# Optimization experiments

Measured on AMD Instinct MI355X. Metric: run time of the kernel, lower is better.

The kernel has to match this reference:

```python
import jax, jax.numpy as jnp
import numpy as np

N = 100_000      # nodes
E = 6_400_000    # directed edges (avg degree 64)
F_IN, H, F_OUT = 128, 16, 64


def setup_inputs() -> dict:
    key = jax.random.key(0)
    k1, k2, k3, k4 = jax.random.split(key, 4)
    x = jax.random.normal(k1, (N, F_IN), dtype=jnp.float32)
    edge_index = jax.random.randint(k2, (2, E), 0, N, dtype=jnp.int32)
    # Glorot-ish init for the two GCNConv weight matrices
    W1 = jax.random.normal(k3, (F_IN, H), dtype=jnp.float32) * (1.0 / np.sqrt(F_IN))
    b1 = jnp.zeros((H,), dtype=jnp.float32)
    W2 = jax.random.normal(k4, (H, F_OUT), dtype=jnp.float32) * (1.0 / np.sqrt(H))
    b2 = jnp.zeros((F_OUT,), dtype=jnp.float32)
    return {"x": x, "edge_index": edge_index, "W1": W1, "b1": b1, "W2": W2, "b2": b2}


def _gcn_conv(x, src, dst, norm, W, b):
    # PyG GCNConv: transform first (small hidden dim), then normalized scatter-add
    h = x @ W                                  # [N, d_out]
    msg = h[src] * norm[:, None]               # gather + scale, [E+N, d_out]
    agg = jax.ops.segment_sum(msg, dst, num_segments=N)
    return agg + b


def reference(x, edge_index, W1, b1, W2, b2):
    src, dst = edge_index[0], edge_index[1]
    # add self-loops (GCNConv default add_self_loops=True)
    loop = jnp.arange(N, dtype=src.dtype)
    src = jnp.concatenate([src, loop])
    dst = jnp.concatenate([dst, loop])
    # symmetric normalization D^{-1/2} (A+I) D^{-1/2}
    deg = jax.ops.segment_sum(jnp.ones(src.shape[0], x.dtype), dst, num_segments=N)
    dinv = jax.lax.rsqrt(jnp.maximum(deg, 1e-12))  # deg >= 1 thanks to self-loops
    norm = dinv[src] * dinv[dst]                   # [E+N]
    h = jax.nn.relu(_gcn_conv(x, src, dst, norm, W1, b1))
    return _gcn_conv(h, src, dst, norm, W2, b2)
```

## Files before the change

### kernel.cpp

```cpp
#include <hip/hip_runtime.h>
#include <hip/hip_fp16.h>

constexpr int NN   = 100000;
constexpr int EE   = 6400000;
constexpr int FIN  = 128;
constexpr int HD   = 16;
constexpr int FOUT = 64;

constexpr int CB     = 9;
constexpr int BUKN   = 1 << CB;
constexpr int NBUK   = (NN + BUKN - 1) >> CB;
constexpr int CHUNK  = 8192;
constexpr int NCHUNK = (EE + CHUNK - 1) / CHUNK;

__global__ __launch_bounds__(256) void zero_chist_kernel(int* __restrict__ chist) {
    chist[threadIdx.x] = 0;
}

__global__ __launch_bounds__(256) void coarse_hist_kernel(const int* __restrict__ dst,
                                                          int* __restrict__ chist) {
    __shared__ int h[256];
    int tid = threadIdx.x;
    h[tid] = 0;
    __syncthreads();
    int stride = gridDim.x * 256;
    for (int i = blockIdx.x * 256 + tid; i < EE / 4; i += stride) {
        int4 d4 = reinterpret_cast<const int4*>(dst)[i];
        atomicAdd(&h[d4.x >> CB], 1);
        atomicAdd(&h[d4.y >> CB], 1);
        atomicAdd(&h[d4.z >> CB], 1);
        atomicAdd(&h[d4.w >> CB], 1);
    }
    __syncthreads();
    if (h[tid]) atomicAdd(&chist[tid], h[tid]);
}

__global__ __launch_bounds__(256) void scan_coarse_kernel(const int* __restrict__ chist,
                                                          int* __restrict__ cofs,
                                                          int* __restrict__ bcur) {
    __shared__ int s[256];
    int tid = threadIdx.x;
    int val = chist[tid];
    s[tid] = val;
    __syncthreads();
    for (int st = 1; st < 256; st <<= 1) {
        int add = (tid >= st) ? s[tid - st] : 0;
        __syncthreads();
        s[tid] += add;
        __syncthreads();
    }
    int excl = s[tid] - val;
    cofs[tid] = excl;
    bcur[tid] = excl;
    if (tid == 255) cofs[256] = s[255];
}

__global__ __launch_bounds__(256) void coarse_scatter_kernel(const int* __restrict__ src,
                                                             const int* __restrict__ dst,
                                                             int* __restrict__ bcur,
                                                             unsigned int* __restrict__ pair) {
    __shared__ int h[256];
    __shared__ int exc[256];
    __shared__ int cur[256];
    __shared__ int gbase[256];
    __shared__ unsigned int stage[CHUNK];
    __shared__ unsigned char binOf[CHUNK];
    int tid = threadIdx.x;
    int e0 = blockIdx.x * CHUNK;
    int n = min(CHUNK, EE - e0);

    h[tid] = 0;
    __syncthreads();
    for (int i = tid; i < n; i += 256) atomicAdd(&h[dst[e0 + i] >> CB], 1);
    __syncthreads();
    {
        int val = h[tid];
        exc[tid] = val;
        __syncthreads();
        for (int st = 1; st < 256; st <<= 1) {
            int add = (tid >= st) ? exc[tid - st] : 0;
            __syncthreads();
            exc[tid] += add;
            __syncthreads();
        }
        exc[tid] -= val;
    }
    cur[tid] = exc[tid];
    gbase[tid] = h[tid] ? atomicAdd(&bcur[tid], h[tid]) : 0;
    __syncthreads();
    for (int i = tid; i < n; i += 256) {
        int d = dst[e0 + i];
        int s = src[e0 + i];
        int b = d >> CB;
        int p = atomicAdd(&cur[b], 1);
        stage[p] = (unsigned int)s | ((unsigned int)(d & (BUKN - 1)) << 20);
        binOf[p] = (unsigned char)b;
    }
    __syncthreads();
    for (int i = tid; i < n; i += 256) {
        int b = binOf[i];
        pair[gbase[b] + (i - exc[b])] = stage[i];
    }
}

__global__ __launch_bounds__(1024) void bucket_build_kernel(const unsigned int* __restrict__ pair,
                                                            const int* __restrict__ cofs,
                                                            int* __restrict__ rowptr,
                                                            int* __restrict__ degi,
                                                            float* __restrict__ dinv,
                                                            int* __restrict__ srcs) {
    __shared__ int h[BUKN];
    __shared__ int sc[BUKN];
    __shared__ int cur[BUKN];
    int tid = threadIdx.x;
    int b = blockIdx.x;
    int lo = cofs[b], hi = cofs[b + 1];

    if (tid < BUKN) h[tid] = 0;
    __syncthreads();
    for (int i = lo + tid; i < hi; i += 1024)
        atomicAdd(&h[(pair[i] >> 20) & (BUKN - 1)], 1);
    __syncthreads();
    if (tid < BUKN) sc[tid] = h[tid];
    __syncthreads();
    for (int st = 1; st < BUKN; st <<= 1) {
        int add = (tid >= st && tid < BUKN) ? sc[tid - st] : 0;
        __syncthreads();
        if (tid < BUKN) sc[tid] += add;
        __syncthreads();
    }
    if (tid < BUKN) {
        int excl = sc[tid] - h[tid];
        int v = (b << CB) + tid;
        cur[tid] = lo + excl;
        if (v < NN) {
            rowptr[v] = lo + excl;
            degi[v]   = h[tid];
            dinv[v]   = rsqrtf((float)(h[tid] + 1));
        }
    }
    __syncthreads();
    for (int i = lo + tid; i < hi; i += 1024) {
        unsigned int pd = pair[i];
        int p = atomicAdd(&cur[(pd >> 20) & (BUKN - 1)], 1);
        srcs[p] = (int)(pd & 0xFFFFFu);
    }
}

__global__ __launch_bounds__(256) void gemm1_kernel(const float* __restrict__ x,
                                                    const float* __restrict__ W1,
                                                    const float* __restrict__ dinv,
                                                    __half* __restrict__ t1) {
    __shared__ float W1s[FIN][HD];
    __shared__ float xs[16][FIN + 1];
    int tid = threadIdx.x;
    int nodeBase = blockIdx.x * 16;

    for (int i = tid; i < FIN * HD; i += 256) W1s[i >> 4][i & 15] = W1[i];
    for (int i = tid; i < 16 * FIN; i += 256) {
        int r = i >> 7, c = i & 127;
        int v = nodeBase + r;
        xs[r][c] = (v < NN) ? x[(long long)v * FIN + c] : 0.0f;
    }
    __syncthreads();

    int r = tid >> 4, j = tid & 15;
    int v = nodeBase + r;
    if (v < NN) {
        float acc = 0.0f;
        #pragma unroll
        for (int k = 0; k < FIN; ++k) acc += xs[r][k] * W1s[k][j];
        t1[v * HD + j] = __float2half(acc * dinv[v]);
    }
}

__global__ __launch_bounds__(256) void gather_relu_kernel(const int* __restrict__ rowptr,
                                                          const int* __restrict__ degi,
                                                          const int* __restrict__ srcs,
                                                          const __half2* __restrict__ t1,
                                                          const float* __restrict__ dinv,
                                                          const float* __restrict__ b1,
                                                          __half2* __restrict__ t2) {
    int gw = (blockIdx.x * 256 + threadIdx.x) >> 6;
    int lane = threadIdx.x & 63;
    int start = rowptr[gw];
    int cnt   = degi[gw];
    int jh  = lane & 7;
    int sub = lane >> 3;
    float2 acc = {0.0f, 0.0f};
    int e = sub;
    for (; e + 24 < cnt; e += 32) {
        int s0 = srcs[start + e];
        int s1 = srcs[start + e + 8];
        int s2 = srcs[start + e + 16];
        int s3 = srcs[start + e + 24];
        float2 v0 = __half22float2(t1[s0 * 8 + jh]);
        float2 v1 = __half22float2(t1[s1 * 8 + jh]);
        float2 v2 = __half22float2(t1[s2 * 8 + jh]);
        float2 v3 = __half22float2(t1[s3 * 8 + jh]);
        acc.x += v0.x + v1.x + v2.x + v3.x;
        acc.y += v0.y + v1.y + v2.y + v3.y;
    }
    for (; e < cnt; e += 8) {
        float2 v = __half22float2(t1[srcs[start + e] * 8 + jh]);
        acc.x += v.x; acc.y += v.y;
    }
    acc.x += __shfl_xor(acc.x, 8);  acc.y += __shfl_xor(acc.y, 8);
    acc.x += __shfl_xor(acc.x, 16); acc.y += __shfl_xor(acc.y, 16);
    acc.x += __shfl_xor(acc.x, 32); acc.y += __shfl_xor(acc.y, 32);
    if (sub == 0) {
        float2 self = __half22float2(t1[gw * 8 + jh]);
        float di = dinv[gw];
        float r0 = fmaxf(di * (acc.x + self.x) + b1[2 * jh], 0.0f) * di;
        float r1 = fmaxf(di * (acc.y + self.y) + b1[2 * jh + 1], 0.0f) * di;
        t2[gw * 8 + jh] = __floats2half2_rn(r0, r1);
    }
}

__global__ __launch_bounds__(256) void gather_gemm2_kernel(const int* __restrict__ rowptr,
                                                           const int* __restrict__ degi,
                                                           const int* __restrict__ srcs,
                                                           const __half2* __restrict__ t2,
                                                           const float* __restrict__ dinv,
                                                           const float* __restrict__ W2,
                                                           const float* __restrict__ b2,
                                                           float* __restrict__ out) {
    __shared__ float W2s[HD][FOUT];
    __shared__ float aS[4][HD];
    int tid = threadIdx.x;
    int wv = tid >> 6;
    int gw = blockIdx.x * 4 + wv;
    int lane = tid & 63;
    int jh  = lane & 7;
    int sub = lane >> 3;

    for (int i = tid; i < HD * FOUT; i += 256) W2s[i >> 6][i & 63] = W2[i];

    int start = rowptr[gw];
    int cnt   = degi[gw];
    float2 acc = {0.0f, 0.0f};
    int e = sub;
    for (; e + 24 < cnt; e += 32) {
        int s0 = srcs[start + e];
        int s1 = srcs[start + e + 8];
        int s2 = srcs[start + e + 16];
        int s3 = srcs[start + e + 24];
        float2 v0 = __half22float2(t2[s0 * 8 + jh]);
        float2 v1 = __half22float2(t2[s1 * 8 + jh]);
        float2 v2 = __half22float2(t2[s2 * 8 + jh]);
        float2 v3 = __half22float2(t2[s3 * 8 + jh]);
        acc.x += v0.x + v1.x + v2.x + v3.x;
        acc.y += v0.y + v1.y + v2.y + v3.y;
    }
    for (; e < cnt; e += 8) {
        float2 v = __half22float2(t2[srcs[start + e] * 8 + jh]);
        acc.x += v.x; acc.y += v.y;
    }
    acc.x += __shfl_xor(acc.x, 8);  acc.y += __shfl_xor(acc.y, 8);
    acc.x += __shfl_xor(acc.x, 16); acc.y += __shfl_xor(acc.y, 16);
    acc.x += __shfl_xor(acc.x, 32); acc.y += __shfl_xor(acc.y, 32);
    if (sub == 0) {
        float2 self = __half22float2(t2[gw * 8 + jh]);
        float di = dinv[gw];
        aS[wv][2 * jh]     = di * (acc.x + self.x);
        aS[wv][2 * jh + 1] = di * (acc.y + self.y);
    }
    __syncthreads();

    int jo = lane;
    float facc = b2[jo];
    #pragma unroll
    for (int k = 0; k < HD; ++k) facc += aS[wv][k] * W2s[k][jo];
    out[(long long)gw * FOUT + jo] = facc;
}

extern "C" void kernel_launch(void* const* d_in, const int* in_sizes, int n_in,
                              void* d_out, int out_size, void* d_ws, size_t ws_size,
                              hipStream_t stream) {
    const float* x  = (const float*)d_in[0];
    const int*   ei = (const int*)d_in[1];
    const float* W1 = (const float*)d_in[2];
    const float* b1 = (const float*)d_in[3];
    const float* W2 = (const float*)d_in[4];
    const float* b2 = (const float*)d_in[5];
    float* out = (float*)d_out;

    const int* src = ei;
    const int* dst = ei + EE;

    int* wsI    = (int*)d_ws;
    int* chist  = wsI;
    int* cofs   = chist + 256;
    int* bcur   = cofs + 288;
    int* rowptr = bcur + 256;
    int* degi   = rowptr + NN;
    float* dinv = (float*)(degi + NN);
    unsigned int* pair = (unsigned int*)(dinv + NN);
    int* srcs   = (int*)(pair + EE);
    __half* t1  = (__half*)(srcs + EE);
    __half* t2  = t1 + NN * HD;

    zero_chist_kernel<<<1, 256, 0, stream>>>(chist);
    coarse_hist_kernel<<<1024, 256, 0, stream>>>(dst, chist);
    scan_coarse_kernel<<<1, 256, 0, stream>>>(chist, cofs, bcur);
    coarse_scatter_kernel<<<NCHUNK, 256, 0, stream>>>(src, dst, bcur, pair);
    bucket_build_kernel<<<NBUK, 1024, 0, stream>>>(pair, cofs, rowptr, degi, dinv, srcs);

    gemm1_kernel<<<(NN + 15) / 16, 256, 0, stream>>>(x, W1, dinv, t1);
    gather_relu_kernel<<<NN / 4, 256, 0, stream>>>(rowptr, degi, srcs,
                                                   (const __half2*)t1, dinv, b1,
                                                   (__half2*)t2);
    gather_gemm2_kernel<<<NN / 4, 256, 0, stream>>>(rowptr, degi, srcs,
                                                    (const __half2*)t2, dinv, W2, b2, out);
}
```

Baseline: 418.7 us.

## Replace atomic bucket allocation with per-chunk histograms and deterministic column scan

Result: faster. 353.5 us (-15.6%).

```diff
diff --git a/kernel.cpp b/kernel.cpp
--- a/kernel.cpp
+++ b/kernel.cpp
@@ -13,34 +13,61 @@
 constexpr int CHUNK  = 8192;
 constexpr int NCHUNK = (EE + CHUNK - 1) / CHUNK;
 
-__global__ __launch_bounds__(256) void zero_chist_kernel(int* __restrict__ chist) {
-    chist[threadIdx.x] = 0;
-}
-
-__global__ __launch_bounds__(256) void coarse_hist_kernel(const int* __restrict__ dst,
-                                                          int* __restrict__ chist) {
+__global__ __launch_bounds__(256) void chunk_hist_kernel(const int* __restrict__ dst,
+                                                         int* __restrict__ histG) {
     __shared__ int h[256];
     int tid = threadIdx.x;
+    int c = blockIdx.x;
+    int e0 = c * CHUNK;
+    int n = min(CHUNK, EE - e0);
     h[tid] = 0;
     __syncthreads();
-    int stride = gridDim.x * 256;
-    for (int i = blockIdx.x * 256 + tid; i < EE / 4; i += stride) {
-        int4 d4 = reinterpret_cast<const int4*>(dst)[i];
-        atomicAdd(&h[d4.x >> CB], 1);
-        atomicAdd(&h[d4.y >> CB], 1);
-        atomicAdd(&h[d4.z >> CB], 1);
-        atomicAdd(&h[d4.w >> CB], 1);
-    }
-    __syncthreads();
-    if (h[tid]) atomicAdd(&chist[tid], h[tid]);
-}
-
-__global__ __launch_bounds__(256) void scan_coarse_kernel(const int* __restrict__ chist,
-                                                          int* __restrict__ cofs,
-                                                          int* __restrict__ bcur) {
+    const int4* dst4 = reinterpret_cast<const int4*>(dst + e0);
+    int n4 = n >> 2;
+    for (int i = tid; i < n4; i += 256) {
+        int4 d = dst4[i];
+        atomicAdd(&h[d.x >> CB], 1);
+        atomicAdd(&h[d.y >> CB], 1);
+        atomicAdd(&h[d.z >> CB], 1);
+        atomicAdd(&h[d.w >> CB], 1);
+    }
+    __syncthreads();
+    histG[c * 256 + tid] = h[tid];
+}
+
+__global__ __launch_bounds__(256) void colscan_kernel(const int* __restrict__ histG,
+                                                      int* __restrict__ offsL,
+                                                      int* __restrict__ totG) {
+    __shared__ int ps[256];
+    int t = threadIdx.x;
+    int b = blockIdx.x;
+    int c0 = 4 * t;
+    int v0 = (c0     < NCHUNK) ? histG[(c0    ) * 256 + b] : 0;
+    int v1 = (c0 + 1 < NCHUNK) ? histG[(c0 + 1) * 256 + b] : 0;
+    int v2 = (c0 + 2 < NCHUNK) ? histG[(c0 + 2) * 256 + b] : 0;
+    int v3 = (c0 + 3 < NCHUNK) ? histG[(c0 + 3) * 256 + b] : 0;
+    int tot = v0 + v1 + v2 + v3;
+    ps[t] = tot;
+    __syncthreads();
+    for (int st = 1; st < 256; st <<= 1) {
+        int add = (t >= st) ? ps[t - st] : 0;
+        __syncthreads();
+        ps[t] += add;
+        __syncthreads();
+    }
+    int base = ps[t] - tot;
+    if (c0     < NCHUNK) offsL[(c0    ) * 256 + b] = base;
+    if (c0 + 1 < NCHUNK) offsL[(c0 + 1) * 256 + b] = base + v0;
+    if (c0 + 2 < NCHUNK) offsL[(c0 + 2) * 256 + b] = base + v0 + v1;
+    if (c0 + 3 < NCHUNK) offsL[(c0 + 3) * 256 + b] = base + v0 + v1 + v2;
+    if (t == 255) totG[b] = ps[255];
+}
+
+__global__ __launch_bounds__(256) void scan_coarse_kernel(const int* __restrict__ totG,
+                                                          int* __restrict__ cofs) {
     __shared__ int s[256];
     int tid = threadIdx.x;
-    int val = chist[tid];
+    int val = totG[tid];
     s[tid] = val;
     __syncthreads();
     for (int st = 1; st < 256; st <<= 1) {
@@ -49,55 +76,65 @@
         s[tid] += add;
         __syncthreads();
     }
-    int excl = s[tid] - val;
-    cofs[tid] = excl;
-    bcur[tid] = excl;
+    cofs[tid] = s[tid] - val;
     if (tid == 255) cofs[256] = s[255];
 }
 
-__global__ __launch_bounds__(256) void coarse_scatter_kernel(const int* __restrict__ src,
+__global__ __launch_bounds__(512) void coarse_scatter_kernel(const int* __restrict__ src,
                                                              const int* __restrict__ dst,
-                                                             int* __restrict__ bcur,
+                                                             const int* __restrict__ histG,
+                                                             const int* __restrict__ offsL,
+                                                             const int* __restrict__ cofs,
                                                              unsigned int* __restrict__ pair) {
-    __shared__ int h[256];
     __shared__ int exc[256];
     __shared__ int cur[256];
     __shared__ int gbase[256];
+    __shared__ int ps[256];
     __shared__ unsigned int stage[CHUNK];
     __shared__ unsigned char binOf[CHUNK];
     int tid = threadIdx.x;
-    int e0 = blockIdx.x * CHUNK;
+    int c = blockIdx.x;
+    int e0 = c * CHUNK;
     int n = min(CHUNK, EE - e0);
 
-    h[tid] = 0;
-    __syncthreads();
-    for (int i = tid; i < n; i += 256) atomicAdd(&h[dst[e0 + i] >> CB], 1);
-    __syncthreads();
-    {
-        int val = h[tid];
-        exc[tid] = val;
-        __syncthreads();
-        for (int st = 1; st < 256; st <<= 1) {
-            int add = (tid >= st) ? exc[tid - st] : 0;
-            __syncthreads();
-            exc[tid] += add;
-            __syncthreads();
-        }
-        exc[tid] -= val;
-    }
-    cur[tid] = exc[tid];
-    gbase[tid] = h[tid] ? atomicAdd(&bcur[tid], h[tid]) : 0;
-    __syncthreads();
-    for (int i = tid; i < n; i += 256) {
-        int d = dst[e0 + i];
-        int s = src[e0 + i];
-        int b = d >> CB;
-        int p = atomicAdd(&cur[b], 1);
-        stage[p] = (unsigned int)s | ((unsigned int)(d & (BUKN - 1)) << 20);
-        binOf[p] = (unsigned char)b;
-    }
-    __syncthreads();
-    for (int i = tid; i < n; i += 256) {
+    int val = 0;
+    if (tid < 256) {
+        val = histG[c * 256 + tid];
+        ps[tid] = val;
+        gbase[tid] = cofs[tid] + offsL[c * 256 + tid];
+    }
+    __syncthreads();
+    for (int st = 1; st < 256; st <<= 1) {
+        int add = (tid >= st && tid < 256) ? ps[tid - st] : 0;
+        __syncthreads();
+        if (tid < 256) ps[tid] += add;
+        __syncthreads();
+    }
+    if (tid < 256) { exc[tid] = ps[tid] - val; cur[tid] = ps[tid] - val; }
+    __syncthreads();
+
+    const int4* dst4 = reinterpret_cast<const int4*>(dst + e0);
+    const int4* src4 = reinterpret_cast<const int4*>(src + e0);
+    int n4 = n >> 2;
+    for (int i = tid; i < n4; i += 512) {
+        int4 d = dst4[i];
+        int4 s = src4[i];
+        int b0 = d.x >> CB, b1 = d.y >> CB, b2 = d.z >> CB, b3 = d.w >> CB;
+        int p0 = atomicAdd(&cur[b0], 1);
+        int p1 = atomicAdd(&cur[b1], 1);
+        int p2 = atomicAdd(&cur[b2], 1);
+        int p3 = atomicAdd(&cur[b3], 1);
+        stage[p0] = (unsigned int)s.x | ((unsigned int)(d.x & (BUKN - 1)) << 20);
+        stage[p1] = (unsigned int)s.y | ((unsigned int)(d.y & (BUKN - 1)) << 20);
+        stage[p2] = (unsigned int)s.z | ((unsigned int)(d.z & (BUKN - 1)) << 20);
+        stage[p3] = (unsigned int)s.w | ((unsigned int)(d.w & (BUKN - 1)) << 20);
+        binOf[p0] = (unsigned char)b0;
+        binOf[p1] = (unsigned char)b1;
+        binOf[p2] = (unsigned char)b2;
+        binOf[p3] = (unsigned char)b3;
+    }
+    __syncthreads();
+    for (int i = tid; i < n; i += 512) {
         int b = binOf[i];
         pair[gbase[b] + (i - exc[b])] = stage[i];
     }
@@ -289,10 +326,11 @@
     const int* dst = ei + EE;
 
     int* wsI    = (int*)d_ws;
-    int* chist  = wsI;
-    int* cofs   = chist + 256;
-    int* bcur   = cofs + 288;
-    int* rowptr = bcur + 256;
+    int* histG  = wsI;
+    int* offsL  = histG + NCHUNK * 256;
+    int* totG   = offsL + NCHUNK * 256;
+    int* cofs   = totG + 256;
+    int* rowptr = cofs + 288;
     int* degi   = rowptr + NN;
     float* dinv = (float*)(degi + NN);
     unsigned int* pair = (unsigned int*)(dinv + NN);
@@ -300,10 +338,10 @@
     __half* t1  = (__half*)(srcs + EE);
     __half* t2  = t1 + NN * HD;
 
-    zero_chist_kernel<<<1, 256, 0, stream>>>(chist);
-    coarse_hist_kernel<<<1024, 256, 0, stream>>>(dst, chist);
-    scan_coarse_kernel<<<1, 256, 0, stream>>>(chist, cofs, bcur);
-    coarse_scatter_kernel<<<NCHUNK, 256, 0, stream>>>(src, dst, bcur, pair);
+    chunk_hist_kernel<<<NCHUNK, 256, 0, stream>>>(dst, histG);
+    colscan_kernel<<<256, 256, 0, stream>>>(histG, offsL, totG);
+    scan_coarse_kernel<<<1, 256, 0, stream>>>(totG, cofs);
+    coarse_scatter_kernel<<<NCHUNK, 512, 0, stream>>>(src, dst, histG, offsL, cofs, pair);
     bucket_build_kernel<<<NBUK, 1024, 0, stream>>>(pair, cofs, rowptr, degi, dinv, srcs);
 
     gemm1_kernel<<<(NN + 15) / 16, 256, 0, stream>>>(x, W1, dinv, t1);
```
